# Optimization experiments

Hardware: AMD Instinct MI355X
Metric: run time of the kernel (lower is better)

## Reference

```python
import jax, jax.numpy as jnp
import numpy as np
from jax import lax

VOCAB = 32000; D = 1024; NL = 4; DI = 2048; S = 16; R = 64; DC = 4
B = 1; L = 1024; EPS = 1e-5


def setup_inputs() -> dict:
    key = jax.random.key(0)
    ks = jax.random.split(key, 16)
    def n(k, shape, s=0.02):
        return jax.random.normal(k, shape, dtype=jnp.float32) * s
    return dict(
        tokens=jax.random.randint(ks[0], (B, L), 0, VOCAB),
        embed=n(ks[1], (VOCAB, D)),
        norm_w=jnp.ones((NL, D), jnp.float32) + n(ks[2], (NL, D)),
        in_proj_w=n(ks[3], (NL, 2 * DI, D)),
        conv_w=n(ks[4], (NL, DI, DC), 0.1),
        conv_b=n(ks[5], (NL, DI)),
        x_proj_w=n(ks[6], (NL, R + 2 * S, DI)),
        dt_proj_w=n(ks[7], (NL, DI, R), 0.1),
        dt_proj_b=n(ks[8], (NL, DI), 0.5),
        A_log=n(ks[9], (NL, DI, S), 0.5),
        D_param=jnp.ones((NL, DI), jnp.float32) + n(ks[10], (NL, DI)),
        out_proj_w=n(ks[11], (NL, D, DI)),
        norm_f_w=jnp.ones((D,), jnp.float32),
        lm_head_w=n(ks[12], (VOCAB, D)),
    )


def _rmsnorm(x, w):
    return x * lax.rsqrt(jnp.mean(x * x, axis=-1, keepdims=True) + EPS) * w


def _mamba_block(x, norm_w, in_w, cw, cb, xw, dtw, dtb, a_log, dp, ow):
    # x: [B, L, D]
    res = x
    x = _rmsnorm(x, norm_w)
    xz = jnp.einsum('bld,ed->ble', x, in_w)      # [B, L, 2*DI]
    u, z = xz[..., :DI], xz[..., DI:]
    # depthwise causal conv over time
    u = jnp.swapaxes(u, 1, 2)                    # [B, DI, L]
    u = lax.conv_general_dilated(u, cw[:, None, :], (1,), [(DC - 1, 0)],
                                 feature_group_count=DI,
                                 dimension_numbers=('NCH', 'OIH', 'NCH'))
    u = jax.nn.silu(u + cb[None, :, None])
    u = jnp.swapaxes(u, 1, 2)                    # [B, L, DI]
    # input-dependent SSM params
    dbc = jnp.einsum('bld,ed->ble', u, xw)       # [B, L, R+2S]
    dt = jax.nn.softplus(jnp.einsum('blr,dr->bld', dbc[..., :R], dtw) + dtb)
    Bm = dbc[..., R:R + S]                       # [B, L, S]
    Cm = dbc[..., R + S:]                        # [B, L, S]
    A = -jnp.exp(a_log)                          # [DI, S]
    dA = jnp.exp(dt[..., None] * A)              # [B, L, DI, S]
    dBu = (dt * u)[..., None] * Bm[:, :, None, :]  # [B, L, DI, S]
    # selective scan over time
    def step(h, inp):
        a_t, b_t, c_t = inp
        h = a_t * h + b_t                        # [B, DI, S]
        y = jnp.einsum('bds,bs->bd', h, c_t)
        return h, y
    h0 = jnp.zeros((x.shape[0], DI, S), x.dtype)
    _, ys = lax.scan(step, h0, (jnp.moveaxis(dA, 1, 0), jnp.moveaxis(dBu, 1, 0), jnp.moveaxis(Cm, 1, 0)))
    y = jnp.moveaxis(ys, 0, 1) + u * dp          # [B, L, DI]
    y = y * jax.nn.silu(z)
    return res + jnp.einsum('bld,od->blo', y, ow)


def reference(tokens, embed, norm_w, in_proj_w, conv_w, conv_b, x_proj_w,
              dt_proj_w, dt_proj_b, A_log, D_param, out_proj_w, norm_f_w, lm_head_w):
    x = embed[tokens]                            # [B, L, D]
    for i in range(NL):
        x = _mamba_block(x, norm_w[i], in_proj_w[i], conv_w[i], conv_b[i],
                         x_proj_w[i], dt_proj_w[i], dt_proj_b[i], A_log[i],
                         D_param[i], out_proj_w[i])
    x = _rmsnorm(x, norm_f_w)
    return jnp.einsum('bld,vd->blv', x, lm_head_w)  # [B, L, VOCAB]
```

## Files before the change

kernel.cpp:

```cpp
#include <hip/hip_runtime.h>
#include <hip/hip_bf16.h>
#include <math.h>


typedef __attribute__((ext_vector_type(8))) short bf16x8;
typedef __attribute__((ext_vector_type(4))) float f32x4;

__device__ __forceinline__ short f2bf(float f) {
  union { float f; unsigned u; } v; v.f = f;
  unsigned u = v.u;
  unsigned r = (u + 0x7FFFu + ((u >> 16) & 1u)) >> 16;
  return (short)r;
}

__device__ __forceinline__ bf16x8 pack8(float4 a, float4 b) {
  bf16x8 r;
  r[0] = f2bf(a.x); r[1] = f2bf(a.y); r[2] = f2bf(a.z); r[3] = f2bf(a.w);
  r[4] = f2bf(b.x); r[5] = f2bf(b.y); r[6] = f2bf(b.z); r[7] = f2bf(b.w);
  return r;
}

__device__ __forceinline__ unsigned cvtpk(float lo, float hi) {
  unsigned r;
  asm("v_cvt_pk_bf16_f32 %0, %1, %2" : "=v"(r) : "v"(lo), "v"(hi));
  return r;
}

__device__ __forceinline__ float softplus_f(float x) {
  return (x > 20.f) ? x : log1pf(__expf(x));
}

__device__ __forceinline__ void gl_lds16(const void* g, void* l) {
  void* gnc = (void*)g;
  __builtin_amdgcn_global_load_lds((__attribute__((address_space(1))) void*)gnc,
                                   (__attribute__((address_space(3))) void*)l, 16, 0, 0);
}

__global__ __launch_bounds__(256) void cvt5_k(const float* __restrict__ s0, unsigned short* __restrict__ d0, int nb0,
                                              const float* __restrict__ s1, unsigned short* __restrict__ d1, int nb1,
                                              const float* __restrict__ s2, unsigned short* __restrict__ d2, int nb2,
                                              const float* __restrict__ s3, unsigned short* __restrict__ d3, int nb3,
                                              const float* __restrict__ s4, unsigned short* __restrict__ d4) {
  int b = blockIdx.x;
  const float* s; unsigned short* d; int lb;
  if (b < nb0) { s = s0; d = d0; lb = b; }
  else if (b < nb0 + nb1) { s = s1; d = d1; lb = b - nb0; }
  else if (b < nb0 + nb1 + nb2) { s = s2; d = d2; lb = b - nb0 - nb1; }
  else if (b < nb0 + nb1 + nb2 + nb3) { s = s3; d = d3; lb = b - nb0 - nb1 - nb2; }
  else { s = s4; d = d4; lb = b - nb0 - nb1 - nb2 - nb3; }
  size_t base = (size_t)lb * 1024;
#pragma unroll
  for (int u = 0; u < 4; ++u) {
    size_t idx = base + u * 256 + threadIdx.x;
    const float4* p = (const float4*)(s + idx * 8);
    float4 a = p[0], bq = p[1];
    uint4 w;
    w.x = cvtpk(a.x, a.y); w.y = cvtpk(a.z, a.w);
    w.z = cvtpk(bq.x, bq.y); w.w = cvtpk(bq.z, bq.w);
    *(uint4*)(d + idx * 8) = w;
  }
}

__global__ __launch_bounds__(256) void embed_rms_k(const int* __restrict__ tok,
                                                   const float* __restrict__ emb,
                                                   const float* __restrict__ w,
                                                   float* __restrict__ x,
                                                   unsigned short* __restrict__ xn16) {
  int l = blockIdx.x;
  int t = tok[l];
  float4 v = ((const float4*)(emb + (size_t)t * 1024))[threadIdx.x];
  ((float4*)(x + (size_t)l * 1024))[threadIdx.x] = v;
  float ss = v.x * v.x + v.y * v.y + v.z * v.z + v.w * v.w;
  ss += __shfl_down(ss, 32); ss += __shfl_down(ss, 16); ss += __shfl_down(ss, 8);
  ss += __shfl_down(ss, 4);  ss += __shfl_down(ss, 2);  ss += __shfl_down(ss, 1);
  __shared__ float wsum[4];
  if ((threadIdx.x & 63) == 0) wsum[threadIdx.x >> 6] = ss;
  __syncthreads();
  float tot = wsum[0] + wsum[1] + wsum[2] + wsum[3];
  float sc = rsqrtf(tot * (1.0f / 1024.0f) + 1e-5f);
  float4 wv = ((const float4*)w)[threadIdx.x];
  ushort4 o;
  o.x = (unsigned short)f2bf(v.x * sc * wv.x);
  o.y = (unsigned short)f2bf(v.y * sc * wv.y);
  o.z = (unsigned short)f2bf(v.z * sc * wv.z);
  o.w = (unsigned short)f2bf(v.w * sc * wv.w);
  *(ushort4*)(xn16 + (size_t)l * 1024 + threadIdx.x * 4) = o;
}

__global__ __launch_bounds__(256) void reduce_op_rms_k(const float* __restrict__ Cp,
                                                       float* __restrict__ x,
                                                       const float* __restrict__ w,
                                                       unsigned short* __restrict__ y16) {
  int l = blockIdx.x;
  int i = l * 256 + threadIdx.x;
  const float4* p0 = (const float4*)Cp;
  const float4* p1 = (const float4*)(Cp + 1048576);
  const float4* p2 = (const float4*)(Cp + 2097152);
  const float4* p3 = (const float4*)(Cp + 3145728);
  float4 a = p0[i], b = p1[i], c = p2[i], d = p3[i];
  float4 xv = ((float4*)x)[i];
  xv.x += a.x + b.x + c.x + d.x;
  xv.y += a.y + b.y + c.y + d.y;
  xv.z += a.z + b.z + c.z + d.z;
  xv.w += a.w + b.w + c.w + d.w;
  ((float4*)x)[i] = xv;
  float ss = xv.x * xv.x + xv.y * xv.y + xv.z * xv.z + xv.w * xv.w;
  ss += __shfl_down(ss, 32); ss += __shfl_down(ss, 16); ss += __shfl_down(ss, 8);
  ss += __shfl_down(ss, 4);  ss += __shfl_down(ss, 2);  ss += __shfl_down(ss, 1);
  __shared__ float wsum[4];
  if ((threadIdx.x & 63) == 0) wsum[threadIdx.x >> 6] = ss;
  __syncthreads();
  float tot = wsum[0] + wsum[1] + wsum[2] + wsum[3];
  float sc = rsqrtf(tot * (1.0f / 1024.0f) + 1e-5f);
  float4 wv = ((const float4*)w)[threadIdx.x];
  ushort4 o;
  o.x = (unsigned short)f2bf(xv.x * sc * wv.x);
  o.y = (unsigned short)f2bf(xv.y * sc * wv.y);
  o.z = (unsigned short)f2bf(xv.z * sc * wv.z);
  o.w = (unsigned short)f2bf(xv.w * sc * wv.w);
  *(ushort4*)(y16 + (size_t)l * 1024 + threadIdx.x * 4) = o;
}

__global__ __launch_bounds__(256) void rmsnorm_k(const float* __restrict__ x,
                                                 const float* __restrict__ w,
                                                 float* __restrict__ y) {
  int l = blockIdx.x;
  const float4* xr = (const float4*)(x + (size_t)l * 1024);
  float4 v = xr[threadIdx.x];
  float ss = v.x * v.x + v.y * v.y + v.z * v.z + v.w * v.w;
  ss += __shfl_down(ss, 32); ss += __shfl_down(ss, 16); ss += __shfl_down(ss, 8);
  ss += __shfl_down(ss, 4);  ss += __shfl_down(ss, 2);  ss += __shfl_down(ss, 1);
  __shared__ float wsum[4];
  if ((threadIdx.x & 63) == 0) wsum[threadIdx.x >> 6] = ss;
  __syncthreads();
  float tot = wsum[0] + wsum[1] + wsum[2] + wsum[3];
  float sc = rsqrtf(tot * (1.0f / 1024.0f) + 1e-5f);
  float4 wv = ((const float4*)w)[threadIdx.x];
  float4 o;
  o.x = v.x * sc * wv.x; o.y = v.y * sc * wv.y;
  o.z = v.z * sc * wv.z; o.w = v.w * sc * wv.w;
  ((float4*)(y + (size_t)l * 1024))[threadIdx.x] = o;
}

__global__ __launch_bounds__(256) void conv_silu_k(const float* __restrict__ xz,
                                                   const float* __restrict__ cw,
                                                   const float* __restrict__ cb,
                                                   float* __restrict__ u,
                                                   unsigned short* __restrict__ u16) {
  int idx = blockIdx.x * 256 + threadIdx.x;
  int d = idx & 2047;
  int l = idx >> 11;
  float acc = cb[d];
#pragma unroll
  for (int j = 0; j < 4; ++j) {
    int ll = l - 3 + j;
    if (ll >= 0) acc = fmaf(xz[(size_t)ll * 4096 + d], cw[d * 4 + j], acc);
  }
  float sig = 1.0f / (1.0f + __expf(-acc));
  float v = acc * sig;
  u[idx] = v;
  if (u16) u16[idx] = (unsigned short)f2bf(v);
}

__global__ __launch_bounds__(256) void gemm16_k(const unsigned short* __restrict__ A, int lda,
                                                const unsigned short* __restrict__ W, int ldw,
                                                const float* __restrict__ addsrc,
                                                const float* __restrict__ spbias,
                                                float* __restrict__ C, int ldc,
                                                unsigned short* __restrict__ C16,
                                                int gx, int N, int K) {
  int total = gridDim.x;
  int lin = blockIdx.x;
  int q = total >> 3, r = total & 7;
  int xcd = lin & 7, idx = lin >> 3;
  int nl = (xcd < r ? xcd * (q + 1) : r * (q + 1) + (xcd - r) * q) + idx;
  const int bm = (nl % gx) << 7;
  const int bn = (nl / gx) << 7;

  const int tid = threadIdx.x;
  const int wid = tid >> 6;
  const int lane = tid & 63;
  const int wm = (wid >> 1) << 6;
  const int wn = (wid & 1) << 6;
  const int fr = lane & 15;
  const int kg = lane >> 4;
  const int srow = lane >> 3;
  const int sch  = lane & 7;
  const int xch  = sch ^ srow;

  __shared__ unsigned short sA[2][8192];
  __shared__ unsigned short sB[2][8192];

  f32x4 acc[4][4];
#pragma unroll
  for (int i = 0; i < 4; ++i)
#pragma unroll
    for (int j = 0; j < 4; ++j) acc[i][j] = (f32x4){0.f, 0.f, 0.f, 0.f};

  auto STAGE = [&](int b, int k0) {
#pragma unroll
    for (int t = 0; t < 4; ++t) {
      int g = (wid << 2) + t;
      int row = (g << 3) + srow;
      const unsigned short* ga = A + (size_t)(bm + row) * lda + k0 + (xch << 3);
      int wrow = bn + row; if (wrow >= N) wrow = N - 1;
      const unsigned short* gw = W + (size_t)wrow * ldw + k0 + (xch << 3);
      gl_lds16(ga, &sA[b][g << 9]);
      gl_lds16(gw, &sB[b][g << 9]);
    }
  };

  auto COMPUTE = [&](int b) {
#pragma unroll
    for (int ks = 0; ks < 2; ++ks) {
      bf16x8 af[4], bw[4];
#pragma unroll
      for (int mi = 0; mi < 4; ++mi) {
        int row = wm + (mi << 4) + fr;
        int xc = ((ks << 2) + kg) ^ (fr & 7);
        af[mi] = *(const bf16x8*)&sA[b][(row << 6) + (xc << 3)];
      }
#pragma unroll
      for (int ni = 0; ni < 4; ++ni) {
        int row = wn + (ni << 4) + fr;
        int xc = ((ks << 2) + kg) ^ (fr & 7);
        bw[ni] = *(const bf16x8*)&sB[b][(row << 6) + (xc << 3)];
      }
#pragma unroll
      for (int mi = 0; mi < 4; ++mi)
#pragma unroll
        for (int ni = 0; ni < 4; ++ni)
          acc[mi][ni] = __builtin_amdgcn_mfma_f32_16x16x32_bf16(af[mi], bw[ni], acc[mi][ni], 0, 0, 0);
    }
  };

  const int nt = K >> 6;
  STAGE(0, 0);
  int cur = 0;
  for (int t = 0; t + 1 < nt; ++t) {
    STAGE(cur ^ 1, (t + 1) << 6);
    asm volatile("s_waitcnt vmcnt(8)" ::: "memory");
    __builtin_amdgcn_s_barrier();
    __builtin_amdgcn_sched_barrier(0);
    COMPUTE(cur);
    __builtin_amdgcn_s_barrier();
    cur ^= 1;
  }
  asm volatile("s_waitcnt vmcnt(0)" ::: "memory");
  __builtin_amdgcn_s_barrier();
  __builtin_amdgcn_sched_barrier(0);
  COMPUTE(cur);

#pragma unroll
  for (int mi = 0; mi < 4; ++mi)
#pragma unroll
    for (int ni = 0; ni < 4; ++ni) {
      int n = bn + wn + (ni << 4) + fr;
      if (n < N) {
#pragma unroll
        for (int i = 0; i < 4; ++i) {
          int m = bm + wm + (mi << 4) + (kg << 2) + i;
          size_t off = (size_t)m * ldc + n;
          float v = acc[mi][ni][i];
          if (addsrc) v += addsrc[off];
          if (spbias) v = softplus_f(v + spbias[n]);
          C[off] = v;
          if (C16) C16[off] = (unsigned short)f2bf(v);
        }
      }
    }
}

__global__ __launch_bounds__(256) void gemm16sk_k(const unsigned short* __restrict__ A, int lda,
                                                  const unsigned short* __restrict__ W, int ldw,
                                                  float* __restrict__ Cp, int ldc,
                                                  int gx, int N, int Kchunk, int Mtot) {
  int total = gridDim.x;
  int lin = blockIdx.x;
  int q = total >> 3, r = total & 7;
  int xcd = lin & 7, idx = lin >> 3;
  int nl = (xcd < r ? xcd * (q + 1) : r * (q + 1) + (xcd - r) * q) + idx;
  const int bm = (nl % gx) << 7;
  const int bn = (nl / gx) << 7;
  const int ksplit = blockIdx.y;
  const int kbase = ksplit * Kchunk;

  const int tid = threadIdx.x;
  const int wid = tid >> 6;
  const int lane = tid & 63;
  const int wm = (wid >> 1) << 6;
  const int wn = (wid & 1) << 6;
  const int fr = lane & 15;
  const int kg = lane >> 4;
  const int srow = lane >> 3;
  const int sch  = lane & 7;
  const int xch  = sch ^ srow;

  __shared__ unsigned short sA[2][8192];
  __shared__ unsigned short sB[2][8192];

  f32x4 acc[4][4];
#pragma unroll
  for (int i = 0; i < 4; ++i)
#pragma unroll
    for (int j = 0; j < 4; ++j) acc[i][j] = (f32x4){0.f, 0.f, 0.f, 0.f};

  auto STAGE = [&](int b, int k0) {
#pragma unroll
    for (int t = 0; t < 4; ++t) {
      int g = (wid << 2) + t;
      int row = (g << 3) + srow;
      const unsigned short* ga = A + (size_t)(bm + row) * lda + k0 + (xch << 3);
      int wrow = bn + row; if (wrow >= N) wrow = N - 1;
      const unsigned short* gw = W + (size_t)wrow * ldw + k0 + (xch << 3);
      gl_lds16(ga, &sA[b][g << 9]);
      gl_lds16(gw, &sB[b][g << 9]);
    }
  };

  auto COMPUTE = [&](int b) {
#pragma unroll
    for (int ks = 0; ks < 2; ++ks) {
      bf16x8 af[4], bw[4];
#pragma unroll
      for (int mi = 0; mi < 4; ++mi) {
        int row = wm + (mi << 4) + fr;
        int xc = ((ks << 2) + kg) ^ (fr & 7);
        af[mi] = *(const bf16x8*)&sA[b][(row << 6) + (xc << 3)];
      }
#pragma unroll
      for (int ni = 0; ni < 4; ++ni) {
        int row = wn + (ni << 4) + fr;
        int xc = ((ks << 2) + kg) ^ (fr & 7);
        bw[ni] = *(const bf16x8*)&sB[b][(row << 6) + (xc << 3)];
      }
#pragma unroll
      for (int mi = 0; mi < 4; ++mi)
#pragma unroll
        for (int ni = 0; ni < 4; ++ni)
          acc[mi][ni] = __builtin_amdgcn_mfma_f32_16x16x32_bf16(af[mi], bw[ni], acc[mi][ni], 0, 0, 0);
    }
  };

  const int nt = Kchunk >> 6;
  STAGE(0, kbase);
  int cur = 0;
  for (int t = 0; t + 1 < nt; ++t) {
    STAGE(cur ^ 1, kbase + ((t + 1) << 6));
    asm volatile("s_waitcnt vmcnt(8)" ::: "memory");
    __builtin_amdgcn_s_barrier();
    __builtin_amdgcn_sched_barrier(0);
    COMPUTE(cur);
    __builtin_amdgcn_s_barrier();
    cur ^= 1;
  }
  asm volatile("s_waitcnt vmcnt(0)" ::: "memory");
  __builtin_amdgcn_s_barrier();
  __builtin_amdgcn_sched_barrier(0);
  COMPUTE(cur);

  float* Cs = Cp + (size_t)ksplit * Mtot * ldc;
#pragma unroll
  for (int mi = 0; mi < 4; ++mi)
#pragma unroll
    for (int ni = 0; ni < 4; ++ni) {
      int n = bn + wn + (ni << 4) + fr;
      if (n < N) {
#pragma unroll
        for (int i = 0; i < 4; ++i) {
          int m = bm + wm + (mi << 4) + (kg << 2) + i;
          Cs[(size_t)m * ldc + n] = acc[mi][ni][i];
        }
      }
    }
}

__global__ __launch_bounds__(256) void reduce_xp_k(const float* __restrict__ Cp,
                                                   float* __restrict__ dbc,
                                                   unsigned short* __restrict__ dbc16) {
  int i = blockIdx.x * 256 + threadIdx.x;
  float v = Cp[i] + Cp[98304 + i] + Cp[2 * 98304 + i] + Cp[3 * 98304 + i];
  dbc[i] = v;
  dbc16[i] = (unsigned short)f2bf(v);
}

__global__ __launch_bounds__(512, 2) void gemm256_k(const unsigned short* __restrict__ A, int lda,
                                                    const unsigned short* __restrict__ W, int ldw,
                                                    float* __restrict__ C, int ldc,
                                                    int gx, int N, int K) {
  int total = gridDim.x;
  int lin = blockIdx.x;
  int q = total >> 3, r = total & 7;
  int xcd = lin & 7, idx = lin >> 3;
  int nl = (xcd < r ? xcd * (q + 1) : r * (q + 1) + (xcd - r) * q) + idx;
  const int bm = (nl % gx) << 8;
  const int bn = (nl / gx) << 8;

  const int tid = threadIdx.x;
  const int wid = tid >> 6;
  const int lane = tid & 63;
  const int wm = (wid >> 2) << 7;
  const int wn = (wid & 3) << 6;
  const int fr = lane & 15;
  const int kg = lane >> 4;
  const int srow = lane >> 3;
  const int sch  = lane & 7;
  const int xch  = sch ^ srow;

  __shared__ unsigned short sA[2][16384];
  __shared__ unsigned short sB[2][16384];

  f32x4 acc[8][4];
#pragma unroll
  for (int i = 0; i < 8; ++i)
#pragma unroll
    for (int j = 0; j < 4; ++j) acc[i][j] = (f32x4){0.f, 0.f, 0.f, 0.f};

  auto STAGE = [&](int b, int k0) {
#pragma unroll
    for (int t = 0; t < 4; ++t) {
      int g = (wid << 2) + t;
      int row = (g << 3) + srow;
      const unsigned short* ga = A + (size_t)(bm + row) * lda + k0 + (xch << 3);
      int wrow = bn + row; if (wrow >= N) wrow = N - 1;
      const unsigned short* gw = W + (size_t)wrow * ldw + k0 + (xch << 3);
      gl_lds16(ga, &sA[b][g << 9]);
      gl_lds16(gw, &sB[b][g << 9]);
    }
  };

  auto COMPUTE = [&](int b) {
#pragma unroll
    for (int ks = 0; ks < 2; ++ks) {
      bf16x8 af[8], bw[4];
#pragma unroll
      for (int mi = 0; mi < 8; ++mi) {
        int row = wm + (mi << 4) + fr;
        int xc = ((ks << 2) + kg) ^ (fr & 7);
        af[mi] = *(const bf16x8*)&sA[b][(row << 6) + (xc << 3)];
      }
#pragma unroll
      for (int ni = 0; ni < 4; ++ni) {
        int row = wn + (ni << 4) + fr;
        int xc = ((ks << 2) + kg) ^ (fr & 7);
        bw[ni] = *(const bf16x8*)&sB[b][(row << 6) + (xc << 3)];
      }
#pragma unroll
      for (int mi = 0; mi < 8; ++mi)
#pragma unroll
        for (int ni = 0; ni < 4; ++ni)
          acc[mi][ni] = __builtin_amdgcn_mfma_f32_16x16x32_bf16(af[mi], bw[ni], acc[mi][ni], 0, 0, 0);
    }
  };

  const int nt = K >> 6;
  STAGE(0, 0);
  int cur = 0;
  for (int t = 0; t + 1 < nt; ++t) {
    STAGE(cur ^ 1, (t + 1) << 6);
    asm volatile("s_waitcnt vmcnt(8)" ::: "memory");
    __builtin_amdgcn_s_barrier();
    __builtin_amdgcn_sched_barrier(0);
    COMPUTE(cur);
    __builtin_amdgcn_s_barrier();
    cur ^= 1;
  }
  asm volatile("s_waitcnt vmcnt(0)" ::: "memory");
  __builtin_amdgcn_s_barrier();
  __builtin_amdgcn_sched_barrier(0);
  COMPUTE(cur);

#pragma unroll
  for (int mi = 0; mi < 8; ++mi)
#pragma unroll
    for (int ni = 0; ni < 4; ++ni) {
      int n = bn + wn + (ni << 4) + fr;
      if (n < N) {
#pragma unroll
        for (int i = 0; i < 4; ++i) {
          int m = bm + wm + (mi << 4) + (kg << 2) + i;
          C[(size_t)m * ldc + n] = acc[mi][ni][i];
        }
      }
    }
}

__global__ __launch_bounds__(256) void gemm_bt_k(const float* __restrict__ A, int lda,
                                                 const float* __restrict__ W, int ldw,
                                                 const float* __restrict__ addsrc,
                                                 float* __restrict__ C, int ldc,
                                                 int N, int K) {
  const int tid  = threadIdx.x;
  const int srow = tid >> 1;
  const int skg  = (tid & 1) << 1;
  const int bm = blockIdx.x << 7;
  const int bn = blockIdx.y << 7;
  const int wid = tid >> 6;
  const int lane = tid & 63;
  const int wm = (wid >> 1) << 6;
  const int wn = (wid & 1) << 6;
  const int fr = lane & 15;
  const int kg = lane >> 4;

  __shared__ bf16x8 lA[4][128];
  __shared__ bf16x8 lB[4][128];

  f32x4 zero4 = {0.f, 0.f, 0.f, 0.f};
  f32x4 acc[4][4];
#pragma unroll
  for (int i = 0; i < 4; ++i)
#pragma unroll
    for (int j = 0; j < 4; ++j) acc[i][j] = zero4;

  const bool wvalid = (bn + srow) < N;
  const float* gA = A + (size_t)(bm + srow) * lda + (skg << 3);
  const float* gW = W + (size_t)(wvalid ? (bn + srow) : 0) * ldw + (skg << 3);

  for (int k0 = 0; k0 < K; k0 += 32) {
    float4 a0 = *(const float4*)(gA + k0);
    float4 a1 = *(const float4*)(gA + k0 + 4);
    float4 a2 = *(const float4*)(gA + k0 + 8);
    float4 a3 = *(const float4*)(gA + k0 + 12);
    float4 w0 = make_float4(0.f, 0.f, 0.f, 0.f), w1 = w0, w2 = w0, w3 = w0;
    if (wvalid) {
      w0 = *(const float4*)(gW + k0);
      w1 = *(const float4*)(gW + k0 + 4);
      w2 = *(const float4*)(gW + k0 + 8);
      w3 = *(const float4*)(gW + k0 + 12);
    }
    __syncthreads();
    lA[skg][srow]     = pack8(a0, a1);
    lA[skg + 1][srow] = pack8(a2, a3);
    lB[skg][srow]     = pack8(w0, w1);
    lB[skg + 1][srow] = pack8(w2, w3);
    __syncthreads();

    bf16x8 af[4], bf_[4];
#pragma unroll
    for (int mi = 0; mi < 4; ++mi) af[mi] = lA[kg][wm + (mi << 4) + fr];
#pragma unroll
    for (int ni = 0; ni < 4; ++ni) bf_[ni] = lB[kg][wn + (ni << 4) + fr];
#pragma unroll
    for (int mi = 0; mi < 4; ++mi)
#pragma unroll
      for (int ni = 0; ni < 4; ++ni)
        acc[mi][ni] = __builtin_amdgcn_mfma_f32_16x16x32_bf16(af[mi], bf_[ni], acc[mi][ni], 0, 0, 0);
  }

#pragma unroll
  for (int mi = 0; mi < 4; ++mi)
#pragma unroll
    for (int ni = 0; ni < 4; ++ni) {
      int n = bn + wn + (ni << 4) + fr;
      if (n < N) {
#pragma unroll
        for (int i = 0; i < 4; ++i) {
          int m = bm + wm + (mi << 4) + (kg << 2) + i;
          size_t off = (size_t)m * ldc + n;
          float v = acc[mi][ni][i];
          if (addsrc) v += addsrc[off];
          C[off] = v;
        }
      }
    }
}

#define NCH 32
#define CHL 32

__global__ __launch_bounds__(256) void scan_p1f_k(const float* __restrict__ dtv,
                                                  const float* __restrict__ u,
                                                  const float* __restrict__ dbc,
                                                  const float* __restrict__ A_log,
                                                  float* __restrict__ Pg,
                                                  float* __restrict__ qg) {
  int tid = threadIdx.x;
  int s = tid & 15, dg = tid >> 4;
  int d = (blockIdx.x << 4) + dg;
  int c = blockIdx.y;
  int l0 = c << 5;
  float A = -__expf(A_log[d * 16 + s]);
  float P = 1.f, q = 0.f;
#pragma unroll 4
  for (int i = 0; i < CHL; ++i) {
    int l = l0 + i;
    size_t rd = (size_t)l * 2048 + d;
    float dt = dtv[rd];
    float dA = __expf(dt * A);
    P *= dA;
    q = fmaf(dA, q, dt * u[rd] * dbc[l * 96 + 64 + s]);
  }
  size_t o = (size_t)c * 32768 + d * 16 + s;
  Pg[o] = P;
  qg[o] = q;
}

__global__ __launch_bounds__(256) void scan_p3f_k(const float* __restrict__ dtv,
                                                  const float* __restrict__ u,
                                                  const float* __restrict__ dbc,
                                                  const float* __restrict__ xz,
                                                  const float* __restrict__ A_log,
                                                  const float* __restrict__ Dp,
                                                  const float* __restrict__ Pg,
                                                  const float* __restrict__ qg,
                                                  unsigned short* __restrict__ y16) {
  int tid = threadIdx.x;
  int s = tid & 15, dg = tid >> 4;
  int d = (blockIdx.x << 4) + dg;
  int c = blockIdx.y;
  int l0 = c << 5;
  float A = -__expf(A_log[d * 16 + s]);
  float dpar = Dp[d];
  float h = 0.f;
  for (int cc = 0; cc < c; ++cc) {
    size_t o = (size_t)cc * 32768 + d * 16 + s;
    h = fmaf(Pg[o], h, qg[o]);
  }
#pragma unroll 4
  for (int i = 0; i < CHL; ++i) {
    int l = l0 + i;
    size_t rd = (size_t)l * 2048 + d;
    float dt = dtv[rd];
    float uv = u[rd];
    float dA = __expf(dt * A);
    h = fmaf(dA, h, dt * uv * dbc[l * 96 + 64 + s]);
    float p = h * dbc[l * 96 + 80 + s];
    p += __shfl_xor(p, 1); p += __shfl_xor(p, 2);
    p += __shfl_xor(p, 4); p += __shfl_xor(p, 8);
    if (s == 0) {
      float zv = xz[(size_t)l * 4096 + 2048 + d];
      float sig = 1.0f / (1.0f + __expf(-zv));
      y16[rd] = (unsigned short)f2bf((p + uv * dpar) * (zv * sig));
    }
  }
}

__global__ __launch_bounds__(256) void scan_p1_k(const float* __restrict__ dtr,
                                                 const float* __restrict__ u,
                                                 const float* __restrict__ dbc,
                                                 const float* __restrict__ A_log,
                                                 const float* __restrict__ dtb,
                                                 float* __restrict__ Pg,
                                                 float* __restrict__ qg) {
  int tid = threadIdx.x;
  int s = tid & 15, dg = tid >> 4;
  int d = (blockIdx.x << 4) + dg;
  int c = blockIdx.y;
  int l0 = c << 5;
  float A = -__expf(A_log[d * 16 + s]);
  float bias = dtb[d];
  float P = 1.f, q = 0.f;
#pragma unroll 4
  for (int i = 0; i < CHL; ++i) {
    int l = l0 + i;
    float dt = softplus_f(dtr[(size_t)l * 2048 + d] + bias);
    float dA = __expf(dt * A);
    P *= dA;
    q = fmaf(dA, q, dt * u[(size_t)l * 2048 + d] * dbc[l * 96 + 64 + s]);
  }
  size_t o = (size_t)c * 32768 + d * 16 + s;
  Pg[o] = P;
  qg[o] = q;
}

__global__ __launch_bounds__(256) void scan_p2_k(const float* __restrict__ Pg,
                                                 const float* __restrict__ qg,
                                                 float* __restrict__ hst) {
  int idx = blockIdx.x * 256 + threadIdx.x;
  float h = 0.f;
#pragma unroll
  for (int c = 0; c < NCH; ++c) {
    size_t o = (size_t)c * 32768 + idx;
    hst[o] = h;
    h = fmaf(Pg[o], h, qg[o]);
  }
}

__global__ __launch_bounds__(256) void scan_p3_k(const float* __restrict__ dtr,
                                                 const float* __restrict__ u,
                                                 const float* __restrict__ dbc,
                                                 const float* __restrict__ xz,
                                                 const float* __restrict__ A_log,
                                                 const float* __restrict__ Dp,
                                                 const float* __restrict__ dtb,
                                                 const float* __restrict__ hst,
                                                 float* __restrict__ y) {
  int tid = threadIdx.x;
  int s = tid & 15, dg = tid >> 4;
  int d = (blockIdx.x << 4) + dg;
  int c = blockIdx.y;
  int l0 = c << 5;
  float A = -__expf(A_log[d * 16 + s]);
  float dpar = Dp[d];
  float bias = dtb[d];
  float h = hst[(size_t)c * 32768 + d * 16 + s];
#pragma unroll 4
  for (int i = 0; i < CHL; ++i) {
    int l = l0 + i;
    size_t rd = (size_t)l * 2048 + d;
    float dt = softplus_f(dtr[rd] + bias);
    float uv = u[rd];
    float dA = __expf(dt * A);
    h = fmaf(dA, h, dt * uv * dbc[l * 96 + 64 + s]);
    float p = h * dbc[l * 96 + 80 + s];
    p += __shfl_xor(p, 1); p += __shfl_xor(p, 2);
    p += __shfl_xor(p, 4); p += __shfl_xor(p, 8);
    if (s == 0) {
      float zv = xz[(size_t)l * 4096 + 2048 + d];
      float sig = 1.0f / (1.0f + __expf(-zv));
      y[rd] = (p + uv * dpar) * (zv * sig);
    }
  }
}

extern "C" void kernel_launch(void* const* d_in, const int* in_sizes, int n_in,
                              void* d_out, int out_size, void* d_ws, size_t ws_size,
                              hipStream_t stream) {
  const int*   tokens = (const int*)d_in[0];
  const float* embed  = (const float*)d_in[1];
  const float* norm_w = (const float*)d_in[2];
  const float* in_w   = (const float*)d_in[3];
  const float* conv_w = (const float*)d_in[4];
  const float* conv_b = (const float*)d_in[5];
  const float* x_w    = (const float*)d_in[6];
  const float* dt_w   = (const float*)d_in[7];
  const float* dt_b   = (const float*)d_in[8];
  const float* A_log  = (const float*)d_in[9];
  const float* D_par  = (const float*)d_in[10];
  const float* out_w  = (const float*)d_in[11];
  const float* normf  = (const float*)d_in[12];
  const float* lm_w   = (const float*)d_in[13];

  float* out = (float*)d_out;
  float* x    = out;
  float* xz   = x    + 1024 * 1024;
  float* u    = xz   + 1024 * 4096;
  float* dtv  = u    + 1024 * 2048;
  float* dbc  = dtv  + 1024 * 2048;
  float* Pg   = dbc  + 1024 * 96;
  float* qg   = Pg   + 32 * 32768;
  float* hst  = qg   + 32 * 32768;
  float* xn_f = hst  + 32 * 32768;
  float* y_f  = xn_f + 1024 * 1024;
  unsigned short* xn16  = (unsigned short*)(y_f + 1024 * 2048);
  unsigned short* u16   = xn16 + 1024 * 1024;
  unsigned short* y16   = u16  + 1024 * 2048;
  unsigned short* dbc16 = y16  + 1024 * 2048;
  float* part_op = (float*)(dbc16 + 1024 * 96);
  float* part_xp = part_op + 4 * 1048576;

  unsigned short* inw16 = (unsigned short*)d_ws;
  unsigned short* oww16 = inw16 + 16777216;
  unsigned short* xw16  = oww16 + 8388608;
  unsigned short* dtw16 = xw16  + 786432;
  unsigned short* lmw16 = dtw16 + 524288;
  unsigned short* xnf16 = lmw16 + 32768000;
  const size_t need = (size_t)(16777216 + 8388608 + 786432 + 524288 + 32768000 + 1048576) * 2;
  const bool fast = ws_size >= need;

  if (fast) {
    cvt5_k<<<7232, 256, 0, stream>>>(in_w, inw16, 2048,
                                     out_w, oww16, 1024,
                                     x_w, xw16, 96,
                                     dt_w, dtw16, 64,
                                     lm_w, lmw16);
    embed_rms_k<<<1024, 256, 0, stream>>>(tokens, embed, norm_w, x, xn16);

    for (int i = 0; i < 4; ++i) {
      gemm16_k<<<256, 256, 0, stream>>>(xn16, 1024, inw16 + (size_t)i * 4194304, 1024,
                                        nullptr, nullptr, xz, 4096, nullptr, 8, 4096, 1024);
      conv_silu_k<<<8192, 256, 0, stream>>>(xz, conv_w + i * 8192, conv_b + i * 2048, u, u16);
      gemm16sk_k<<<dim3(8, 4), 256, 0, stream>>>(u16, 2048, xw16 + (size_t)i * 196608, 2048,
                                                 part_xp, 96, 8, 96, 512, 1024);
      reduce_xp_k<<<384, 256, 0, stream>>>(part_xp, dbc, dbc16);
      gemm16_k<<<128, 256, 0, stream>>>(dbc16, 96, dtw16 + (size_t)i * 131072, 64,
                                        nullptr, dt_b + i * 2048, dtv, 2048, nullptr, 8, 2048, 64);
      scan_p1f_k<<<dim3(128, NCH), 256, 0, stream>>>(dtv, u, dbc, A_log + i * 32768, Pg, qg);
      scan_p3f_k<<<dim3(128, NCH), 256, 0, stream>>>(dtv, u, dbc, xz, A_log + i * 32768,
                                                     D_par + i * 2048, Pg, qg, y16);
      gemm16sk_k<<<dim3(64, 4), 256, 0, stream>>>(y16, 2048, oww16 + (size_t)i * 2097152, 2048,
                                                  part_op, 1024, 8, 1024, 512, 1024);
      const float* wn = (i < 3) ? (norm_w + (i + 1) * 1024) : normf;
      unsigned short* yn = (i < 3) ? xn16 : xnf16;
      reduce_op_rms_k<<<1024, 256, 0, stream>>>(part_op, x, wn, yn);
    }

    gemm256_k<<<500, 512, 0, stream>>>(xnf16, 1024, lmw16, 1024, out, 32000, 4, 32000, 1024);
  } else {
    float* xnf_f = (float*)d_ws;
    embed_rms_k<<<1024, 256, 0, stream>>>(tokens, embed, norm_w, x, xn16);
    for (int i = 0; i < 4; ++i) {
      rmsnorm_k<<<1024, 256, 0, stream>>>(x, norm_w + i * 1024, xn_f);
      gemm_bt_k<<<dim3(8, 32), 256, 0, stream>>>(xn_f, 1024, in_w + (size_t)i * 4194304, 1024,
                                                 nullptr, xz, 4096, 4096, 1024);
      conv_silu_k<<<8192, 256, 0, stream>>>(xz, conv_w + i * 8192, conv_b + i * 2048, u, nullptr);
      gemm_bt_k<<<dim3(8, 1), 256, 0, stream>>>(u, 2048, x_w + (size_t)i * 196608, 2048,
                                                nullptr, dbc, 96, 96, 2048);
      gemm_bt_k<<<dim3(8, 16), 256, 0, stream>>>(dbc, 96, dt_w + (size_t)i * 131072, 64,
                                                 nullptr, dtv, 2048, 2048, 64);
      scan_p1_k<<<dim3(128, NCH), 256, 0, stream>>>(dtv, u, dbc, A_log + i * 32768,
                                                    dt_b + i * 2048, Pg, qg);
      scan_p2_k<<<128, 256, 0, stream>>>(Pg, qg, hst);
      scan_p3_k<<<dim3(128, NCH), 256, 0, stream>>>(dtv, u, dbc, xz, A_log + i * 32768,
                                                    D_par + i * 2048, dt_b + i * 2048, hst, y_f);
      gemm_bt_k<<<dim3(8, 8), 256, 0, stream>>>(y_f, 2048, out_w + (size_t)i * 2097152, 2048,
                                                x, x, 1024, 1024, 2048);
    }
    rmsnorm_k<<<1024, 256, 0, stream>>>(x, normf, xnf_f);
    gemm_bt_k<<<dim3(8, 250), 256, 0, stream>>>(xnf_f, 1024, lm_w, 1024,
                                                nullptr, out, 32000, 32000, 1024);
  }
}
```

Before: 955.0 us.

## Fuse dt projection into scan kernels and retile LM-head GEMM with triple buffering

The separate dt-projection GEMM is removed. Each scan pass now recomputes dt for its 32-step chunk and 16 channels in shared memory, from bf16 dbc and dt weights, with the softplus applied there. This avoids writing and reading the full L×DI dt tensor, at the cost of doing that small GEMM twice (once in p1 and once in p3). The LM-head GEMM moves to 128x256 tiles with a 3-stage LDS pipeline and doubles its grid to 1000 blocks, trading more reloads of the weight tile for lower per-block register use and better latency hiding.

After: 894.3 us. -6.4%, faster.

```diff
diff --git a/kernel.cpp b/kernel.cpp
--- a/kernel.cpp
+++ b/kernel.cpp
@@ -11,6 +11,12 @@
   unsigned u = v.u;
   unsigned r = (u + 0x7FFFu + ((u >> 16) & 1u)) >> 16;
   return (short)r;
+}
+
+__device__ __forceinline__ float bf2f(short x) {
+  union { unsigned u; float f; } v;
+  v.u = ((unsigned)(unsigned short)x) << 16;
+  return v.f;
 }
 
 __device__ __forceinline__ bf16x8 pack8(float4 a, float4 b) {
@@ -384,7 +390,7 @@
   dbc16[i] = (unsigned short)f2bf(v);
 }
 
-__global__ __launch_bounds__(512, 2) void gemm256_k(const unsigned short* __restrict__ A, int lda,
+__global__ __launch_bounds__(512, 2) void gemm_lm_k(const unsigned short* __restrict__ A, int lda,
                                                     const unsigned short* __restrict__ W, int ldw,
                                                     float* __restrict__ C, int ldc,
                                                     int gx, int N, int K) {
@@ -393,13 +399,13 @@
   int q = total >> 3, r = total & 7;
   int xcd = lin & 7, idx = lin >> 3;
   int nl = (xcd < r ? xcd * (q + 1) : r * (q + 1) + (xcd - r) * q) + idx;
-  const int bm = (nl % gx) << 8;
+  const int bm = (nl % gx) << 7;
   const int bn = (nl / gx) << 8;
 
   const int tid = threadIdx.x;
   const int wid = tid >> 6;
   const int lane = tid & 63;
-  const int wm = (wid >> 2) << 7;
+  const int wm = (wid >> 2) << 6;
   const int wn = (wid & 3) << 6;
   const int fr = lane & 15;
   const int kg = lane >> 4;
@@ -407,34 +413,40 @@
   const int sch  = lane & 7;
   const int xch  = sch ^ srow;
 
-  __shared__ unsigned short sA[2][16384];
-  __shared__ unsigned short sB[2][16384];
-
-  f32x4 acc[8][4];
-#pragma unroll
-  for (int i = 0; i < 8; ++i)
+  __shared__ unsigned short sA[3][8192];
+  __shared__ unsigned short sB[3][16384];
+
+  f32x4 acc[4][4];
+#pragma unroll
+  for (int i = 0; i < 4; ++i)
 #pragma unroll
     for (int j = 0; j < 4; ++j) acc[i][j] = (f32x4){0.f, 0.f, 0.f, 0.f};
 
-  auto STAGE = [&](int b, int k0) {
-#pragma unroll
-    for (int t = 0; t < 4; ++t) {
-      int g = (wid << 2) + t;
-      int row = (g << 3) + srow;
-      const unsigned short* ga = A + (size_t)(bm + row) * lda + k0 + (xch << 3);
-      int wrow = bn + row; if (wrow >= N) wrow = N - 1;
-      const unsigned short* gw = W + (size_t)wrow * ldw + k0 + (xch << 3);
-      gl_lds16(ga, &sA[b][g << 9]);
-      gl_lds16(gw, &sB[b][g << 9]);
+  auto STAGE = [&](int b, int t) {
+    int k0 = t << 6;
+#pragma unroll
+    for (int i = 0; i < 6; ++i) {
+      int g = wid * 6 + i;
+      if (g < 16) {
+        int row = (g << 3) + srow;
+        const unsigned short* ga = A + (size_t)(bm + row) * lda + k0 + (xch << 3);
+        gl_lds16(ga, &sA[b][g << 9]);
+      } else {
+        int gb = g - 16;
+        int row = (gb << 3) + srow;
+        int wrow = bn + row; if (wrow >= N) wrow = N - 1;
+        const unsigned short* gw = W + (size_t)wrow * ldw + k0 + (xch << 3);
+        gl_lds16(gw, &sB[b][gb << 9]);
+      }
     }
   };
 
   auto COMPUTE = [&](int b) {
 #pragma unroll
     for (int ks = 0; ks < 2; ++ks) {
-      bf16x8 af[8], bw[4];
-#pragma unroll
-      for (int mi = 0; mi < 8; ++mi) {
+      bf16x8 af[4], bw[4];
+#pragma unroll
+      for (int mi = 0; mi < 4; ++mi) {
         int row = wm + (mi << 4) + fr;
         int xc = ((ks << 2) + kg) ^ (fr & 7);
         af[mi] = *(const bf16x8*)&sA[b][(row << 6) + (xc << 3)];
@@ -446,7 +458,7 @@
         bw[ni] = *(const bf16x8*)&sB[b][(row << 6) + (xc << 3)];
       }
 #pragma unroll
-      for (int mi = 0; mi < 8; ++mi)
+      for (int mi = 0; mi < 4; ++mi)
 #pragma unroll
         for (int ni = 0; ni < 4; ++ni)
           acc[mi][ni] = __builtin_amdgcn_mfma_f32_16x16x32_bf16(af[mi], bw[ni], acc[mi][ni], 0, 0, 0);
@@ -454,24 +466,31 @@
   };
 
   const int nt = K >> 6;
-  STAGE(0, 0);
-  int cur = 0;
-  for (int t = 0; t + 1 < nt; ++t) {
-    STAGE(cur ^ 1, (t + 1) << 6);
-    asm volatile("s_waitcnt vmcnt(8)" ::: "memory");
+  STAGE(0, 0); STAGE(1, 1); STAGE(2, 2);
+
+  int bi = 0;
+  for (int t = 0; t <= nt - 3; ++t) {
+    asm volatile("s_waitcnt vmcnt(12)" ::: "memory");
     __builtin_amdgcn_s_barrier();
     __builtin_amdgcn_sched_barrier(0);
-    COMPUTE(cur);
+    COMPUTE(bi);
     __builtin_amdgcn_s_barrier();
-    cur ^= 1;
-  }
+    if (t + 3 < nt) STAGE(bi, t + 3);
+    bi = (bi == 2) ? 0 : bi + 1;
+  }
+  asm volatile("s_waitcnt vmcnt(6)" ::: "memory");
+  __builtin_amdgcn_s_barrier();
+  __builtin_amdgcn_sched_barrier(0);
+  COMPUTE(bi);
+  __builtin_amdgcn_s_barrier();
+  bi = (bi == 2) ? 0 : bi + 1;
   asm volatile("s_waitcnt vmcnt(0)" ::: "memory");
   __builtin_amdgcn_s_barrier();
   __builtin_amdgcn_sched_barrier(0);
-  COMPUTE(cur);
-
-#pragma unroll
-  for (int mi = 0; mi < 8; ++mi)
+  COMPUTE(bi);
+
+#pragma unroll
+  for (int mi = 0; mi < 4; ++mi)
 #pragma unroll
     for (int ni = 0; ni < 4; ++ni) {
       int n = bn + wn + (ni << 4) + fr;
@@ -567,8 +586,11 @@
 
 #define NCH 32
 #define CHL 32
-
-__global__ __launch_bounds__(256) void scan_p1f_k(const float* __restrict__ dtv,
+#define SDP 68
+
+__global__ __launch_bounds__(256) void scan_p1f_k(const unsigned short* __restrict__ dbc16,
+                                                  const unsigned short* __restrict__ dtw16,
+                                                  const float* __restrict__ dtb,
                                                   const float* __restrict__ u,
                                                   const float* __restrict__ dbc,
                                                   const float* __restrict__ A_log,
@@ -576,26 +598,60 @@
                                                   float* __restrict__ qg) {
   int tid = threadIdx.x;
   int s = tid & 15, dg = tid >> 4;
-  int d = (blockIdx.x << 4) + dg;
+  int d0 = blockIdx.x << 4;
+  int d = d0 + dg;
   int c = blockIdx.y;
   int l0 = c << 5;
+
+  __shared__ float sdbc[32][SDP];
+  __shared__ float sdtw[16][SDP];
+  __shared__ float sdt[32][16];
+
+  {
+    int row = tid >> 3, ch = tid & 7;
+    bf16x8 v = *(const bf16x8*)&dbc16[(size_t)(l0 + row) * 96 + ch * 8];
+#pragma unroll
+    for (int j = 0; j < 8; ++j) sdbc[row][ch * 8 + j] = bf2f(v[j]);
+    if (tid < 128) {
+      bf16x8 w = *(const bf16x8*)&dtw16[(size_t)(d0 + row) * 64 + ch * 8];
+#pragma unroll
+      for (int j = 0; j < 8; ++j) sdtw[row][ch * 8 + j] = bf2f(w[j]);
+    }
+  }
+  __syncthreads();
+  {
+    int ll = tid >> 4, dd = tid & 15;
+    float a0 = 0.f, a1 = 0.f;
+#pragma unroll 8
+    for (int k = 0; k < 64; ++k) {
+      float wv = sdtw[dd][k];
+      a0 = fmaf(sdbc[ll][k], wv, a0);
+      a1 = fmaf(sdbc[ll + 16][k], wv, a1);
+    }
+    float bias = dtb[d0 + dd];
+    sdt[ll][dd]      = softplus_f(a0 + bias);
+    sdt[ll + 16][dd] = softplus_f(a1 + bias);
+  }
+  __syncthreads();
+
   float A = -__expf(A_log[d * 16 + s]);
   float P = 1.f, q = 0.f;
 #pragma unroll 4
   for (int i = 0; i < CHL; ++i) {
     int l = l0 + i;
-    size_t rd = (size_t)l * 2048 + d;
-    float dt = dtv[rd];
+    float dt = sdt[i][dg];
     float dA = __expf(dt * A);
     P *= dA;
-    q = fmaf(dA, q, dt * u[rd] * dbc[l * 96 + 64 + s]);
+    q = fmaf(dA, q, dt * u[(size_t)l * 2048 + d] * dbc[l * 96 + 64 + s]);
   }
   size_t o = (size_t)c * 32768 + d * 16 + s;
   Pg[o] = P;
   qg[o] = q;
 }
 
-__global__ __launch_bounds__(256) void scan_p3f_k(const float* __restrict__ dtv,
+__global__ __launch_bounds__(256) void scan_p3f_k(const unsigned short* __restrict__ dbc16,
+                                                  const unsigned short* __restrict__ dtw16,
+                                                  const float* __restrict__ dtb,
                                                   const float* __restrict__ u,
                                                   const float* __restrict__ dbc,
                                                   const float* __restrict__ xz,
@@ -606,9 +662,42 @@
                                                   unsigned short* __restrict__ y16) {
   int tid = threadIdx.x;
   int s = tid & 15, dg = tid >> 4;
-  int d = (blockIdx.x << 4) + dg;
+  int d0 = blockIdx.x << 4;
+  int d = d0 + dg;
   int c = blockIdx.y;
   int l0 = c << 5;
+
+  __shared__ float sdbc[32][SDP];
+  __shared__ float sdtw[16][SDP];
+  __shared__ float sdt[32][16];
+
+  {
+    int row = tid >> 3, ch = tid & 7;
+    bf16x8 v = *(const bf16x8*)&dbc16[(size_t)(l0 + row) * 96 + ch * 8];
+#pragma unroll
+    for (int j = 0; j < 8; ++j) sdbc[row][ch * 8 + j] = bf2f(v[j]);
+    if (tid < 128) {
+      bf16x8 w = *(const bf16x8*)&dtw16[(size_t)(d0 + row) * 64 + ch * 8];
+#pragma unroll
+      for (int j = 0; j < 8; ++j) sdtw[row][ch * 8 + j] = bf2f(w[j]);
+    }
+  }
+  __syncthreads();
+  {
+    int ll = tid >> 4, dd = tid & 15;
+    float a0 = 0.f, a1 = 0.f;
+#pragma unroll 8
+    for (int k = 0; k < 64; ++k) {
+      float wv = sdtw[dd][k];
+      a0 = fmaf(sdbc[ll][k], wv, a0);
+      a1 = fmaf(sdbc[ll + 16][k], wv, a1);
+    }
+    float bias = dtb[d0 + dd];
+    sdt[ll][dd]      = softplus_f(a0 + bias);
+    sdt[ll + 16][dd] = softplus_f(a1 + bias);
+  }
+  __syncthreads();
+
   float A = -__expf(A_log[d * 16 + s]);
   float dpar = Dp[d];
   float h = 0.f;
@@ -620,7 +709,7 @@
   for (int i = 0; i < CHL; ++i) {
     int l = l0 + i;
     size_t rd = (size_t)l * 2048 + d;
-    float dt = dtv[rd];
+    float dt = sdt[i][dg];
     float uv = u[rd];
     float dA = __expf(dt * A);
     h = fmaf(dA, h, dt * uv * dbc[l * 96 + 64 + s]);
@@ -773,11 +862,13 @@
       gemm16sk_k<<<dim3(8, 4), 256, 0, stream>>>(u16, 2048, xw16 + (size_t)i * 196608, 2048,
                                                  part_xp, 96, 8, 96, 512, 1024);
       reduce_xp_k<<<384, 256, 0, stream>>>(part_xp, dbc, dbc16);
-      gemm16_k<<<128, 256, 0, stream>>>(dbc16, 96, dtw16 + (size_t)i * 131072, 64,
-                                        nullptr, dt_b + i * 2048, dtv, 2048, nullptr, 8, 2048, 64);
-      scan_p1f_k<<<dim3(128, NCH), 256, 0, stream>>>(dtv, u, dbc, A_log + i * 32768, Pg, qg);
-      scan_p3f_k<<<dim3(128, NCH), 256, 0, stream>>>(dtv, u, dbc, xz, A_log + i * 32768,
-                                                     D_par + i * 2048, Pg, qg, y16);
+      scan_p1f_k<<<dim3(128, NCH), 256, 0, stream>>>(dbc16, dtw16 + (size_t)i * 131072,
+                                                     dt_b + i * 2048, u, dbc,
+                                                     A_log + i * 32768, Pg, qg);
+      scan_p3f_k<<<dim3(128, NCH), 256, 0, stream>>>(dbc16, dtw16 + (size_t)i * 131072,
+                                                     dt_b + i * 2048, u, dbc, xz,
+                                                     A_log + i * 32768, D_par + i * 2048,
+                                                     Pg, qg, y16);
       gemm16sk_k<<<dim3(64, 4), 256, 0, stream>>>(y16, 2048, oww16 + (size_t)i * 2097152, 2048,
                                                   part_op, 1024, 8, 1024, 512, 1024);
       const float* wn = (i < 3) ? (norm_w + (i + 1) * 1024) : normf;
@@ -785,7 +876,7 @@
       reduce_op_rms_k<<<1024, 256, 0, stream>>>(part_op, x, wn, yn);
     }
 
-    gemm256_k<<<500, 512, 0, stream>>>(xnf16, 1024, lmw16, 1024, out, 32000, 4, 32000, 1024);
+    gemm_lm_k<<<1000, 512, 0, stream>>>(xnf16, 1024, lmw16, 1024, out, 32000, 8, 32000, 1024);
   } else {
     float* xnf_f = (float*)d_ws;
     embed_rms_k<<<1024, 256, 0, stream>>>(tokens, embed, norm_w, x, xn16);
```
